# Kernel optimization log

Measured on AMD Instinct MI355X. Metric: run time of the kernel, lower is better.

Reference implementation:

```python
import jax, jax.numpy as jnp
import numpy as np

N_NODES = 100000
N_EDGES = 1600000
IN_F = 256
OUT_F = 128


def setup_inputs() -> dict:
    key = jax.random.key(0)
    k1, k2, k3, k4, k5 = jax.random.split(key, 5)
    x = jax.random.normal(k1, (N_NODES, IN_F), dtype=jnp.float32)
    edge_rows = jax.random.randint(k2, (N_EDGES,), 0, N_NODES, dtype=jnp.int32)
    edge_cols = jax.random.randint(k3, (N_EDGES,), 0, N_NODES, dtype=jnp.int32)
    edge_vals = jax.random.uniform(k4, (N_EDGES,), dtype=jnp.float32)
    # glorot init for weight, zeros for bias (matches reset_parameters)
    limit = float(np.sqrt(6.0 / (IN_F + OUT_F)))
    weight = jax.random.uniform(k5, (IN_F, OUT_F), dtype=jnp.float32,
                                minval=-limit, maxval=limit)
    bias = jnp.zeros((OUT_F,), dtype=jnp.float32)
    return {"x": x, "edge_rows": edge_rows, "edge_cols": edge_cols,
            "edge_vals": edge_vals, "weight": weight, "bias": bias}


def reference(x, edge_rows, edge_cols, edge_vals, weight, bias):
    # dense projection: [N, in] @ [in, out] -> [N, out]
    h = x @ weight
    # spmm(adj, h): out[r] = sum_{edges e with row r} vals[e] * h[col[e]]
    msgs = edge_vals[:, None] * h[edge_cols]          # [E, out]
    agg = jax.ops.segment_sum(msgs, edge_rows, num_segments=N_NODES)
    return agg + bias
```

## Files before the change

kernel.cpp:

```cpp
#include <hip/hip_runtime.h>


typedef __attribute__((ext_vector_type(8))) short short8;
typedef __attribute__((ext_vector_type(4))) float floatx4;
typedef __attribute__((ext_vector_type(2))) int intv2;

#define WT_K 264
#define GM_NODES 128
#define BSHIFT 6
#define BROWS 64
#define CAP 192
#define CSH 4
#define OVFCAP 65536
#define XCC_GETREG_IMM 6164

static __device__ __forceinline__ uint f2bf(float x) {
  uint u = __float_as_uint(x);
  return (u + 0x7fffu + ((u >> 16) & 1u)) >> 16;
}

__global__ __launch_bounds__(256) void conv_w(const float* __restrict__ w,
                                              ushort* __restrict__ wt) {
  const int f = blockIdx.x;
  const int k = threadIdx.x;
  wt[f * WT_K + k] = (ushort)f2bf(w[k * 128 + f]);
}

__global__ __launch_bounds__(256) void gemm_mfma(const float* __restrict__ x,
                                                 const ushort* __restrict__ wt,
                                                 ushort* __restrict__ h,
                                                 int n_nodes) {
  __shared__ ushort lw[128 * WT_K];
  __shared__ ushort xa[GM_NODES * 40];
  const int t = threadIdx.x;
  const int lane = t & 63;
  const int wq = t >> 6;
  const int quad = lane >> 4;
  const int l15 = lane & 15;
  const int row0 = blockIdx.x * GM_NODES;

  {
    const uint4* src = (const uint4*)wt;
    uint4* dst = (uint4*)lw;
    for (int i = t; i < (128 * WT_K * 2) / 16; i += 256) dst[i] = src[i];
  }

  floatx4 acc[2][8];
#pragma unroll
  for (int nt = 0; nt < 2; ++nt)
#pragma unroll
    for (int mt = 0; mt < 8; ++mt) acc[nt][mt] = (floatx4){0.f, 0.f, 0.f, 0.f};

  float4 cur[4];
#pragma unroll
  for (int i = 0; i < 4; ++i) {
    const int idx = i * 256 + t;
    const int row = idx >> 3, kq = idx & 7;
    const int gr = row0 + row;
    cur[i] = (gr < n_nodes) ? *(const float4*)&x[(size_t)gr * 256 + kq * 4]
                            : make_float4(0.f, 0.f, 0.f, 0.f);
  }

  for (int kc = 0; kc < 8; ++kc) {
#pragma unroll
    for (int i = 0; i < 4; ++i) {
      const int idx = i * 256 + t;
      const int row = idx >> 3, kq = idx & 7;
      uint2 p;
      p.x = f2bf(cur[i].x) | (f2bf(cur[i].y) << 16);
      p.y = f2bf(cur[i].z) | (f2bf(cur[i].w) << 16);
      *(uint2*)&xa[row * 40 + kq * 4] = p;
    }
    __syncthreads();

    float4 nxt[4];
    if (kc < 7) {
#pragma unroll
      for (int i = 0; i < 4; ++i) {
        const int idx = i * 256 + t;
        const int row = idx >> 3, kq = idx & 7;
        const int gr = row0 + row;
        nxt[i] = (gr < n_nodes)
                     ? *(const float4*)&x[(size_t)gr * 256 + (kc + 1) * 32 + kq * 4]
                     : make_float4(0.f, 0.f, 0.f, 0.f);
      }
    }

    short8 bfr[2];
    bfr[0] = *(const short8*)&xa[(wq * 32 + l15) * 40 + quad * 8];
    bfr[1] = *(const short8*)&xa[(wq * 32 + 16 + l15) * 40 + quad * 8];
#pragma unroll
    for (int mt = 0; mt < 8; ++mt) {
      const short8 afr =
          *(const short8*)&lw[(mt * 16 + l15) * WT_K + kc * 32 + quad * 8];
      acc[0][mt] = __builtin_amdgcn_mfma_f32_16x16x32_bf16(afr, bfr[0],
                                                           acc[0][mt], 0, 0, 0);
      acc[1][mt] = __builtin_amdgcn_mfma_f32_16x16x32_bf16(afr, bfr[1],
                                                           acc[1][mt], 0, 0, 0);
    }
    __syncthreads();
#pragma unroll
    for (int i = 0; i < 4; ++i) cur[i] = nxt[i];
  }

#pragma unroll
  for (int nt = 0; nt < 2; ++nt) {
    const int node = row0 + wq * 32 + nt * 16 + l15;
    if (node < n_nodes) {
#pragma unroll
      for (int mt = 0; mt < 8; ++mt) {
        uint2 p;
        p.x = f2bf(acc[nt][mt][0]) | (f2bf(acc[nt][mt][1]) << 16);
        p.y = f2bf(acc[nt][mt][2]) | (f2bf(acc[nt][mt][3]) << 16);
        *(uint2*)&h[(size_t)node * 128 + mt * 16 + quad * 4] = p;
      }
    }
  }
}

__global__ __launch_bounds__(256) void fill_xcd(
    const int* __restrict__ erows, const int* __restrict__ ecols,
    const float* __restrict__ evals, int* __restrict__ cursors,
    int2* __restrict__ bcv, int* __restrict__ ovf_cnt,
    int4* __restrict__ ovf, int n_edges, int nb) {
  int i = blockIdx.x * 256 + threadIdx.x;
  if (i >= n_edges) return;
  const int xcd = (int)(__builtin_amdgcn_s_getreg(XCC_GETREG_IMM)) & 7;
  const int r = __builtin_nontemporal_load(&erows[i]);
  const int c = __builtin_nontemporal_load(&ecols[i]);
  const float v = __builtin_nontemporal_load(&evals[i]);
  const int reg = xcd * nb + (r >> BSHIFT);
  const int pos = atomicAdd(&cursors[reg << CSH], 1);
  if (pos < CAP) {
    int2 p;
    p.x = c | ((r & (BROWS - 1)) << 17);
    p.y = __float_as_int(v);
    bcv[(size_t)reg * CAP + pos] = p;
  } else {
    int op = atomicAdd(ovf_cnt, 1);
    if (op < OVFCAP) {
      int4 q; q.x = r; q.y = c; q.z = __float_as_int(v); q.w = 0;
      ovf[op] = q;
    }
  }
}

__global__ __launch_bounds__(256) void sort_gather(
    const ushort* __restrict__ h, const int* __restrict__ cursors,
    const int2* __restrict__ bcv, const float* __restrict__ bias,
    float* __restrict__ out, int n_nodes, int nb) {
  __shared__ int2 buf[8 * CAP];
  __shared__ int cnt[BROWS], start[BROWS], cur[BROWS];
  __shared__ int scnt[8];
  const int b = blockIdx.x;
  const int t = threadIdx.x;
  if (t < 8) scnt[t] = min(cursors[(t * nb + b) << CSH], CAP);
  if (t < BROWS) cnt[t] = 0;
  __syncthreads();

#pragma unroll
  for (int x = 0; x < 8; ++x) {
    const int n = scnt[x];
    const int2* src = &bcv[(size_t)(x * nb + b) * CAP];
    for (int i = t; i < n; i += 256) atomicAdd(&cnt[((uint)src[i].x) >> 17], 1);
  }
  __syncthreads();

  if (t < BROWS) {
    int c = cnt[t];
    int s = c;
#pragma unroll
    for (int off = 1; off < 64; off <<= 1) {
      int u = __shfl_up(s, off, 64);
      if (t >= off) s += u;
    }
    start[t] = s - c;
    cur[t] = s - c;
  }
  __syncthreads();

#pragma unroll
  for (int x = 0; x < 8; ++x) {
    const int n = scnt[x];
    const intv2* src = (const intv2*)&bcv[(size_t)(x * nb + b) * CAP];
    for (int i = t; i < n; i += 256) {
      intv2 rr = __builtin_nontemporal_load(&src[i]);
      int2 rec; rec.x = rr[0]; rec.y = rr[1];
      int pos = atomicAdd(&cur[((uint)rec.x) >> 17], 1);
      buf[pos] = rec;
    }
  }
  __syncthreads();

  const int lane = t & 63;
  const int w = t >> 6;
  const float2 bv = ((const float2*)bias)[lane];
  for (int rr = w * 16; rr < w * 16 + 16; ++rr) {
    const int node = b * BROWS + rr;
    if (node >= n_nodes) break;
    float2 acc = bv;
    int p = start[rr];
    const int p1 = start[rr] + cnt[rr];
    for (; p + 4 <= p1; p += 4) {
      int2 e0 = buf[p + 0];
      int2 e1 = buf[p + 1];
      int2 e2 = buf[p + 2];
      int2 e3 = buf[p + 3];
      uint u0 = ((const uint*)(h + (size_t)(e0.x & 0x1FFFF) * 128))[lane];
      uint u1 = ((const uint*)(h + (size_t)(e1.x & 0x1FFFF) * 128))[lane];
      uint u2 = ((const uint*)(h + (size_t)(e2.x & 0x1FFFF) * 128))[lane];
      uint u3 = ((const uint*)(h + (size_t)(e3.x & 0x1FFFF) * 128))[lane];
      float v0 = __int_as_float(e0.y), v1 = __int_as_float(e1.y);
      float v2 = __int_as_float(e2.y), v3 = __int_as_float(e3.y);
      acc.x += v0 * __uint_as_float(u0 << 16);
      acc.y += v0 * __uint_as_float(u0 & 0xffff0000u);
      acc.x += v1 * __uint_as_float(u1 << 16);
      acc.y += v1 * __uint_as_float(u1 & 0xffff0000u);
      acc.x += v2 * __uint_as_float(u2 << 16);
      acc.y += v2 * __uint_as_float(u2 & 0xffff0000u);
      acc.x += v3 * __uint_as_float(u3 << 16);
      acc.y += v3 * __uint_as_float(u3 & 0xffff0000u);
    }
    for (; p < p1; ++p) {
      int2 ev = buf[p];
      float v = __int_as_float(ev.y);
      uint u = ((const uint*)(h + (size_t)(ev.x & 0x1FFFF) * 128))[lane];
      acc.x += v * __uint_as_float(u << 16);
      acc.y += v * __uint_as_float(u & 0xffff0000u);
    }
    ((float2*)(out + (size_t)node * 128))[lane] = acc;
  }
}

__global__ __launch_bounds__(256) void ovf_scatter(
    const ushort* __restrict__ h, const int* __restrict__ ovf_cnt,
    const int4* __restrict__ ovf, float* __restrict__ out) {
  const int n = min(*ovf_cnt, OVFCAP);
  const int lane = threadIdx.x & 63;
  const int wid = (blockIdx.x * 256 + threadIdx.x) >> 6;
  const int nw = gridDim.x * 4;
  for (int e = wid; e < n; e += nw) {
    int4 rec = ovf[e];
    float v = __int_as_float(rec.z);
    uint u = ((const uint*)(h + (size_t)rec.y * 128))[lane];
    float* op = out + (size_t)rec.x * 128 + lane * 2;
    atomicAdd(op, v * __uint_as_float(u << 16));
    atomicAdd(op + 1, v * __uint_as_float(u & 0xffff0000u));
  }
}

__global__ __launch_bounds__(256) void init_bias(float* __restrict__ out,
                                                 const float* __restrict__ bias,
                                                 int n4) {
  int i = blockIdx.x * 256 + threadIdx.x;
  if (i < n4) {
    float4 b = ((const float4*)bias)[i & 31];
    ((float4*)out)[i] = b;
  }
}

__global__ __launch_bounds__(256) void scatter_edges(
    const ushort* __restrict__ h, const int* __restrict__ erows,
    const int* __restrict__ ecols, const float* __restrict__ evals,
    float* __restrict__ out, int n_edges) {
  int e = blockIdx.x * 4 + (threadIdx.x >> 6);
  if (e >= n_edges) return;
  int lane = threadIdx.x & 63;
  int row = erows[e];
  int col = ecols[e];
  float v = evals[e];
  uint u = ((const uint*)(h + (size_t)col * 128))[lane];
  float* op = out + (size_t)row * 128 + lane * 2;
  atomicAdd(op, v * __uint_as_float(u << 16));
  atomicAdd(op + 1, v * __uint_as_float(u & 0xffff0000u));
}

extern "C" void kernel_launch(void* const* d_in, const int* in_sizes, int n_in,
                              void* d_out, int out_size, void* d_ws, size_t ws_size,
                              hipStream_t stream) {
  const float* x     = (const float*)d_in[0];
  const int*   erows = (const int*)d_in[1];
  const int*   ecols = (const int*)d_in[2];
  const float* evals = (const float*)d_in[3];
  const float* w     = (const float*)d_in[4];
  const float* bias  = (const float*)d_in[5];
  float* out = (float*)d_out;

  const int n_nodes = in_sizes[0] / 256;
  const int n_edges = in_sizes[1];
  const int nb_buckets = (n_nodes + BROWS - 1) >> BSHIFT;
  const int nb8 = nb_buckets * 8;

  char* ws = (char*)d_ws;
  size_t off = 0;
  ushort* h  = (ushort*)(ws + off);  off += ((size_t)n_nodes * 128 * 2 + 255) & ~255ull;
  ushort* wt = (ushort*)(ws + off);  off += ((size_t)128 * WT_K * 2 + 255) & ~255ull;
  const size_t cur_ints = (((size_t)nb8) << CSH) + 16;
  int* cursors = (int*)(ws + off);   off += (cur_ints * 4 + 255) & ~255ull;
  int2* bcv    = (int2*)(ws + off);  off += ((size_t)nb8 * CAP * 8 + 255) & ~255ull;
  int4* ovf    = (int4*)(ws + off);  off += (size_t)OVFCAP * 16;
  const bool bucket_ok = (off <= ws_size) && (n_nodes <= (1 << 17));
  int* ovf_cnt = cursors + (((size_t)nb8) << CSH);

  conv_w<<<128, 256, 0, stream>>>(w, wt);
  const int gemm_blocks = (n_nodes + GM_NODES - 1) / GM_NODES;
  gemm_mfma<<<gemm_blocks, 256, 0, stream>>>(x, wt, h, n_nodes);

  if (bucket_ok) {
    hipMemsetAsync(cursors, 0, cur_ints * 4, stream);
    const int eblocks = (n_edges + 255) / 256;
    fill_xcd<<<eblocks, 256, 0, stream>>>(erows, ecols, evals, cursors, bcv,
                                          ovf_cnt, ovf, n_edges, nb_buckets);
    sort_gather<<<nb_buckets, 256, 0, stream>>>(h, cursors, bcv, bias, out,
                                                n_nodes, nb_buckets);
    ovf_scatter<<<32, 256, 0, stream>>>(h, ovf_cnt, ovf, out);
  } else {
    const int n4 = out_size / 4;
    init_bias<<<(n4 + 255) / 256, 256, 0, stream>>>(out, bias, n4);
    scatter_edges<<<(n_edges + 3) / 4, 256, 0, stream>>>(h, erows, ecols, evals,
                                                         out, n_edges);
  }
}
```

Measured before the change: 333.6 us.

## Fold cursor zeroing into conv_w, batch fill per thread, widen gather unroll

The separate hipMemsetAsync on the cursor array is removed and the zeroing is done inside the conv_w kernel, saving one launch/memset on the stream. fill_xcd now handles four edges per thread with all loads issued before the atomics, raising memory-level parallelism and cutting the block count. The sort_gather inner loop is unrolled to eight edges with two independent accumulators to expose more outstanding h loads and shorten the FMA dependency chain. The risks are higher register pressure and a slightly different floating-point summation order.

```diff
diff --git a/kernel.cpp b/kernel.cpp
--- a/kernel.cpp
+++ b/kernel.cpp
@@ -20,10 +20,14 @@
 }
 
 __global__ __launch_bounds__(256) void conv_w(const float* __restrict__ w,
-                                              ushort* __restrict__ wt) {
+                                              ushort* __restrict__ wt,
+                                              int* __restrict__ cursors,
+                                              int n_ints) {
   const int f = blockIdx.x;
   const int k = threadIdx.x;
   wt[f * WT_K + k] = (ushort)f2bf(w[k * 128 + f]);
+  for (int i = blockIdx.x * 256 + threadIdx.x; i < n_ints; i += 128 * 256)
+    cursors[i] = 0;
 }
 
 __global__ __launch_bounds__(256) void gemm_mfma(const float* __restrict__ x,
@@ -123,24 +127,36 @@
     const float* __restrict__ evals, int* __restrict__ cursors,
     int2* __restrict__ bcv, int* __restrict__ ovf_cnt,
     int4* __restrict__ ovf, int n_edges, int nb) {
-  int i = blockIdx.x * 256 + threadIdx.x;
-  if (i >= n_edges) return;
+  const int base = blockIdx.x * 1024 + threadIdx.x;
   const int xcd = (int)(__builtin_amdgcn_s_getreg(XCC_GETREG_IMM)) & 7;
-  const int r = __builtin_nontemporal_load(&erows[i]);
-  const int c = __builtin_nontemporal_load(&ecols[i]);
-  const float v = __builtin_nontemporal_load(&evals[i]);
-  const int reg = xcd * nb + (r >> BSHIFT);
-  const int pos = atomicAdd(&cursors[reg << CSH], 1);
-  if (pos < CAP) {
-    int2 p;
-    p.x = c | ((r & (BROWS - 1)) << 17);
-    p.y = __float_as_int(v);
-    bcv[(size_t)reg * CAP + pos] = p;
-  } else {
-    int op = atomicAdd(ovf_cnt, 1);
-    if (op < OVFCAP) {
-      int4 q; q.x = r; q.y = c; q.z = __float_as_int(v); q.w = 0;
-      ovf[op] = q;
+  int rr[4], cc[4];
+  float vv[4];
+#pragma unroll
+  for (int j = 0; j < 4; ++j) {
+    const int i = base + j * 256;
+    if (i < n_edges) {
+      rr[j] = __builtin_nontemporal_load(&erows[i]);
+      cc[j] = __builtin_nontemporal_load(&ecols[i]);
+      vv[j] = __builtin_nontemporal_load(&evals[i]);
+    }
+  }
+#pragma unroll
+  for (int j = 0; j < 4; ++j) {
+    const int i = base + j * 256;
+    if (i >= n_edges) continue;
+    const int reg = xcd * nb + (rr[j] >> BSHIFT);
+    const int pos = atomicAdd(&cursors[reg << CSH], 1);
+    if (pos < CAP) {
+      int2 p;
+      p.x = cc[j] | ((rr[j] & (BROWS - 1)) << 17);
+      p.y = __float_as_int(vv[j]);
+      bcv[(size_t)reg * CAP + pos] = p;
+    } else {
+      int op = atomicAdd(ovf_cnt, 1);
+      if (op < OVFCAP) {
+        int4 q; q.x = rr[j]; q.y = cc[j]; q.z = __float_as_int(vv[j]); q.w = 0;
+        ovf[op] = q;
+      }
     }
   }
 }
@@ -198,37 +214,59 @@
   for (int rr = w * 16; rr < w * 16 + 16; ++rr) {
     const int node = b * BROWS + rr;
     if (node >= n_nodes) break;
-    float2 acc = bv;
+    float2 acca = bv;
+    float2 accb = make_float2(0.f, 0.f);
     int p = start[rr];
     const int p1 = start[rr] + cnt[rr];
-    for (; p + 4 <= p1; p += 4) {
+    for (; p + 8 <= p1; p += 8) {
       int2 e0 = buf[p + 0];
       int2 e1 = buf[p + 1];
       int2 e2 = buf[p + 2];
       int2 e3 = buf[p + 3];
+      int2 e4 = buf[p + 4];
+      int2 e5 = buf[p + 5];
+      int2 e6 = buf[p + 6];
+      int2 e7 = buf[p + 7];
       uint u0 = ((const uint*)(h + (size_t)(e0.x & 0x1FFFF) * 128))[lane];
       uint u1 = ((const uint*)(h + (size_t)(e1.x & 0x1FFFF) * 128))[lane];
       uint u2 = ((const uint*)(h + (size_t)(e2.x & 0x1FFFF) * 128))[lane];
       uint u3 = ((const uint*)(h + (size_t)(e3.x & 0x1FFFF) * 128))[lane];
+      uint u4 = ((const uint*)(h + (size_t)(e4.x & 0x1FFFF) * 128))[lane];
+      uint u5 = ((const uint*)(h + (size_t)(e5.x & 0x1FFFF) * 128))[lane];
+      uint u6 = ((const uint*)(h + (size_t)(e6.x & 0x1FFFF) * 128))[lane];
+      uint u7 = ((const uint*)(h + (size_t)(e7.x & 0x1FFFF) * 128))[lane];
       float v0 = __int_as_float(e0.y), v1 = __int_as_float(e1.y);
       float v2 = __int_as_float(e2.y), v3 = __int_as_float(e3.y);
-      acc.x += v0 * __uint_as_float(u0 << 16);
-      acc.y += v0 * __uint_as_float(u0 & 0xffff0000u);
-      acc.x += v1 * __uint_as_float(u1 << 16);
-      acc.y += v1 * __uint_as_float(u1 & 0xffff0000u);
-      acc.x += v2 * __uint_as_float(u2 << 16);
-      acc.y += v2 * __uint_as_float(u2 & 0xffff0000u);
-      acc.x += v3 * __uint_as_float(u3 << 16);
-      acc.y += v3 * __uint_as_float(u3 & 0xffff0000u);
+      float v4 = __int_as_float(e4.y), v5 = __int_as_float(e5.y);
+      float v6 = __int_as_float(e6.y), v7 = __int_as_float(e7.y);
+      acca.x += v0 * __uint_as_float(u0 << 16);
+      acca.y += v0 * __uint_as_float(u0 & 0xffff0000u);
+      accb.x += v1 * __uint_as_float(u1 << 16);
+      accb.y += v1 * __uint_as_float(u1 & 0xffff0000u);
+      acca.x += v2 * __uint_as_float(u2 << 16);
+      acca.y += v2 * __uint_as_float(u2 & 0xffff0000u);
+      accb.x += v3 * __uint_as_float(u3 << 16);
+      accb.y += v3 * __uint_as_float(u3 & 0xffff0000u);
+      acca.x += v4 * __uint_as_float(u4 << 16);
+      acca.y += v4 * __uint_as_float(u4 & 0xffff0000u);
+      accb.x += v5 * __uint_as_float(u5 << 16);
+      accb.y += v5 * __uint_as_float(u5 & 0xffff0000u);
+      acca.x += v6 * __uint_as_float(u6 << 16);
+      acca.y += v6 * __uint_as_float(u6 & 0xffff0000u);
+      accb.x += v7 * __uint_as_float(u7 << 16);
+      accb.y += v7 * __uint_as_float(u7 & 0xffff0000u);
     }
     for (; p < p1; ++p) {
       int2 ev = buf[p];
       float v = __int_as_float(ev.y);
       uint u = ((const uint*)(h + (size_t)(ev.x & 0x1FFFF) * 128))[lane];
-      acc.x += v * __uint_as_float(u << 16);
-      acc.y += v * __uint_as_float(u & 0xffff0000u);
-    }
-    ((float2*)(out + (size_t)node * 128))[lane] = acc;
+      acca.x += v * __uint_as_float(u << 16);
+      acca.y += v * __uint_as_float(u & 0xffff0000u);
+    }
+    float2 accf;
+    accf.x = acca.x + accb.x;
+    accf.y = acca.y + accb.y;
+    ((float2*)(out + (size_t)node * 128))[lane] = accf;
   }
 }
 
@@ -302,13 +340,13 @@
   const bool bucket_ok = (off <= ws_size) && (n_nodes <= (1 << 17));
   int* ovf_cnt = cursors + (((size_t)nb8) << CSH);
 
-  conv_w<<<128, 256, 0, stream>>>(w, wt);
+  const int zero_ints = bucket_ok ? (int)cur_ints : 0;
+  conv_w<<<128, 256, 0, stream>>>(w, wt, cursors, zero_ints);
   const int gemm_blocks = (n_nodes + GM_NODES - 1) / GM_NODES;
   gemm_mfma<<<gemm_blocks, 256, 0, stream>>>(x, wt, h, n_nodes);
 
   if (bucket_ok) {
-    hipMemsetAsync(cursors, 0, cur_ints * 4, stream);
-    const int eblocks = (n_edges + 255) / 256;
+    const int eblocks = (n_edges + 1023) / 1024;
     fill_xcd<<<eblocks, 256, 0, stream>>>(erows, ecols, evals, cursors, bcv,
                                           ovf_cnt, ovf, n_edges, nb_buckets);
     sort_gather<<<nb_buckets, 256, 0, stream>>>(h, cursors, bcv, bias, out,
```

New measurement: 334.6 us. No clear change (+0.3%).
